# Performance work log

Measured on AMD Instinct MI355X. Metric: run time of the kernel, lower is better.

The kernel has to match this reference:

```python
import jax, jax.numpy as jnp
import numpy as np

B, H, W, CIN = 16, 64, 64, 64
KWH, COUT, NSAMPLE = 3, 128, 8


def setup_inputs() -> dict:
    key = jax.random.key(0)
    k1, k2, k3, k4 = jax.random.split(key, 4)
    x = jax.random.normal(k1, (B, H, W, CIN), dtype=jnp.float32)
    mu = jax.random.normal(k2, (KWH, KWH, CIN, COUT), dtype=jnp.float32)
    logstd = jax.random.normal(k3, (KWH, KWH, CIN, COUT), dtype=jnp.float32)
    noise = jax.random.normal(k4, (NSAMPLE, KWH, KWH, CIN, COUT), dtype=jnp.float32)
    return {"x": x, "mu": mu, "logstd": logstd, "noise": noise}


def reference(x, mu, logstd, noise):
    # Sampled kernels: [nsample, kh, kw, cin, cout]
    kernels = mu[None] + noise * jnp.exp(logstd)[None]

    def conv_one(k):
        y = jax.lax.conv_general_dilated(
            x, k, window_strides=(1, 1), padding='SAME',
            dimension_numbers=('NHWC', 'HWIO', 'NHWC'))
        return jax.nn.elu(y)

    # [nsample, B, H, W, cout] -> [B, H, W, nsample, cout]
    out = jax.vmap(conv_one)(kernels)
    return jnp.transpose(out, (1, 2, 3, 0, 4))
```

## Files before the change

### kernel.cpp

```cpp
#include <hip/hip_runtime.h>
#include <hip/hip_bf16.h>

typedef __attribute__((ext_vector_type(8))) short short8;
typedef __attribute__((ext_vector_type(8))) unsigned short ushort8;
typedef __attribute__((ext_vector_type(4))) float floatx4;

#define AS_STRIDE 72

#define KERF_BYTES (1024 * 576 * 2)

__global__ void prep_k(const float* __restrict__ x,
                       const float* __restrict__ mu,
                       const float* __restrict__ logstd,
                       const float* __restrict__ noise,
                       __hip_bfloat16* __restrict__ kerF,
                       __hip_bfloat16* __restrict__ xpad) {
  const int bx = blockIdx.x;
  const int tid = threadIdx.x;
  if (bx >= 72) {
    int i = (bx - 72) * 256 + tid;
    int row = i >> 3, seg = i & 7;
    int b = row / 4356;
    int rem = row - b * 4356;
    int hp = rem / 66, wp = rem - (rem / 66) * 66;
    int h = hp - 1, w = wp - 1;
    ushort8 val = {0, 0, 0, 0, 0, 0, 0, 0};
    if ((unsigned)h < 64u && (unsigned)w < 64u) {
      const float* src = x + ((((size_t)b * 64 + h) * 64 + w) << 6) + (seg << 3);
      float4 v0 = *(const float4*)src;
      float4 v1 = *(const float4*)(src + 4);
      val[0] = __bfloat16_as_ushort(__float2bfloat16(v0.x));
      val[1] = __bfloat16_as_ushort(__float2bfloat16(v0.y));
      val[2] = __bfloat16_as_ushort(__float2bfloat16(v0.z));
      val[3] = __bfloat16_as_ushort(__float2bfloat16(v0.w));
      val[4] = __bfloat16_as_ushort(__float2bfloat16(v1.x));
      val[5] = __bfloat16_as_ushort(__float2bfloat16(v1.y));
      val[6] = __bfloat16_as_ushort(__float2bfloat16(v1.z));
      val[7] = __bfloat16_as_ushort(__float2bfloat16(v1.w));
    }
    *(ushort8*)(xpad + ((size_t)row << 6) + (seg << 3)) = val;
  } else {
    const int s = bx / 9, tap = bx % 9;
    const float* mu_p = mu + tap * 8192;
    const float* ls_p = logstd + tap * 8192;
    const float* nz_p = noise + (s * 9 + tap) * 8192;
    for (int f = tid; f < 1024; f += 256) {
      int khalf = f >> 9;
      int nz = (f >> 6) & 7;
      int lane = f & 63;
      int co = ((nz >> 2) << 6) + (lane & 15) * 4 + (nz & 3);
      int ci0 = khalf * 32 + ((lane >> 4) & 3) * 8;
      short8 frag;
#pragma unroll
      for (int j = 0; j < 8; ++j) {
        int idx = (ci0 + j) * 128 + co;
        float v = mu_p[idx] + nz_p[idx] * expf(ls_p[idx]);
        frag[j] = (short)__bfloat16_as_ushort(__float2bfloat16(v));
      }
      *(short8*)(kerF + ((size_t)((s * 18 + tap * 2 + khalf) * 8 + nz) * 64 + lane) * 8) = frag;
    }
  }
}

__global__ __launch_bounds__(256, 3)
void conv_elu_k(const __hip_bfloat16* __restrict__ xpad,
                const __hip_bfloat16* __restrict__ kerF,
                float* __restrict__ out) {
  __shared__ __hip_bfloat16 As[4 * 66 * AS_STRIDE];

  const int tid = threadIdx.x;
  const int lane = tid & 63;
  const int lane15 = tid & 15;
  const int quad = (tid >> 4) & 3;
  const int wave = tid >> 6;
  const int n_tile = blockIdx.x & 7;
  const int mt_base = blockIdx.x >> 3;

  const int row_sel = wave >> 1;
  const int nz0sel = wave & 1;

  const __hip_bfloat16* bBase =
      kerF + (size_t)n_tile * 18 * 8 * 64 * 8 + (nz0sel << 2) * 512 + lane * 8;
  const __hip_bfloat16* aRowBase =
      As + (row_sel * 66 + lane15) * AS_STRIDE + quad * 8;

  short8 aE[4], aO[4], bE[4], bO[4];

  auto loadB = [&](short8* dst, const __hip_bfloat16* p) {
#pragma unroll
    for (int ni = 0; ni < 4; ++ni)
      dst[ni] = *(const short8*)(p + ni * 512);
  };
  auto loadA = [&](short8* dst, const __hip_bfloat16* row, int khalfOff) {
#pragma unroll
    for (int mi = 0; mi < 4; ++mi)
      dst[mi] = *(const short8*)(row + khalfOff + mi * 16 * AS_STRIDE);
  };

#pragma unroll 1
  for (int it = 0; it < 4; ++it) {
    const int mt = mt_base + (it << 7);
    const int b = mt >> 5;
    const int h0 = (mt & 31) << 1;

    const __hip_bfloat16* xbase = xpad + (((size_t)(b * 66 + h0) * 66) << 6);
    for (int c = tid; c < 2112; c += 256) {
      ushort8 v = *(const ushort8*)(xbase + ((size_t)c << 3));
      int r = c / 528;
      int cc = c - r * 528;
      int j = cc >> 3;
      int ci = (cc & 7) << 3;
      *(ushort8*)&As[(r * 66 + j) * AS_STRIDE + ci] = v;
    }

    floatx4 acc[4][4] = {};
    const __hip_bfloat16* bPtr = bBase;
    const __hip_bfloat16* aRow = aRowBase;

    __syncthreads();

    auto mfmaStep = [&](short8 (&a)[4], short8 (&bb)[4]) {
#pragma unroll
      for (int mi = 0; mi < 4; ++mi)
#pragma unroll
        for (int ni = 0; ni < 4; ++ni)
          acc[mi][ni] = __builtin_amdgcn_mfma_f32_16x16x32_bf16(
              a[mi], bb[ni], acc[mi][ni], 0, 0, 0);
    };

    loadB(bE, bPtr);
    loadA(aE, aRow, 0);
    int kw = 0;
#pragma unroll 1
    for (int tap = 0; tap < 8; ++tap) {
      loadB(bO, bPtr + 4096);
      loadA(aO, aRow, 32);
      mfmaStep(aE, bE);
      bPtr += 8192;
      aRow += AS_STRIDE;
      if (++kw == 3) { kw = 0; aRow += 63 * AS_STRIDE; }
      loadB(bE, bPtr);
      loadA(aE, aRow, 0);
      mfmaStep(aO, bO);
    }
    loadB(bO, bPtr + 4096);
    loadA(aO, aRow, 32);
    mfmaStep(aE, bE);
    mfmaStep(aO, bO);

    const int h = h0 + row_sel;
    float* outp = out + (size_t)((b * 64 + h) * 64) * 1024 +
                  (size_t)(n_tile * 128 + (nz0sel << 6) + (lane15 << 2));
#pragma unroll
    for (int mi = 0; mi < 4; ++mi) {
#pragma unroll
      for (int r = 0; r < 4; ++r) {
        int w = mi * 16 + quad * 4 + r;
        float4 v;
        float e0 = acc[mi][0][r];
        float e1 = acc[mi][1][r];
        float e2 = acc[mi][2][r];
        float e3 = acc[mi][3][r];
        v.x = e0 > 0.f ? e0 : __expf(e0) - 1.f;
        v.y = e1 > 0.f ? e1 : __expf(e1) - 1.f;
        v.z = e2 > 0.f ? e2 : __expf(e2) - 1.f;
        v.w = e3 > 0.f ? e3 : __expf(e3) - 1.f;
        *(float4*)(outp + (size_t)w * 1024) = v;
      }
    }

    if (it < 3) __syncthreads();
  }
}

extern "C" void kernel_launch(void* const* d_in, const int* in_sizes, int n_in,
                              void* d_out, int out_size, void* d_ws, size_t ws_size,
                              hipStream_t stream) {
  const float* x      = (const float*)d_in[0];
  const float* mu     = (const float*)d_in[1];
  const float* logstd = (const float*)d_in[2];
  const float* noise  = (const float*)d_in[3];
  float* out = (float*)d_out;
  __hip_bfloat16* kerF = (__hip_bfloat16*)d_ws;
  __hip_bfloat16* xpad = (__hip_bfloat16*)((char*)d_ws + KERF_BYTES);

  prep_k<<<2250, 256, 0, stream>>>(x, mu, logstd, noise, kerF, xpad);
  conv_elu_k<<<1024, 256, 0, stream>>>(xpad, kerF, out);
}
```

Baseline: 341.5 us.

## Stage padded input tiles via global_load_lds and prefetch next tile under epilogue

The padded input buffer now stores each pixel with a 72-element stride, so a tile can be copied straight into LDS with direct global-to-LDS 16-byte loads and no register round trip or index remapping. The next tile's load is issued before the ELU/store epilogue so it overlaps with output writes. The B-fragment loop is rewritten with triple-buffered registers to prefetch B one half-tap further ahead. In exchange the prep kernel writes about 12% more bytes, the tile load moves more data including padding, and register pressure rises.

```diff
diff --git a/kernel.cpp b/kernel.cpp
--- a/kernel.cpp
+++ b/kernel.cpp
@@ -8,6 +8,8 @@
 #define AS_STRIDE 72
 
 #define KERF_BYTES (1024 * 576 * 2)
+#define XPAD_PIX (16 * 66 * 66)
+#define XPAD_SEGS (XPAD_PIX * 9)
 
 __global__ void prep_k(const float* __restrict__ x,
                        const float* __restrict__ mu,
@@ -19,26 +21,28 @@
   const int tid = threadIdx.x;
   if (bx >= 72) {
     int i = (bx - 72) * 256 + tid;
-    int row = i >> 3, seg = i & 7;
-    int b = row / 4356;
-    int rem = row - b * 4356;
-    int hp = rem / 66, wp = rem - (rem / 66) * 66;
-    int h = hp - 1, w = wp - 1;
-    ushort8 val = {0, 0, 0, 0, 0, 0, 0, 0};
-    if ((unsigned)h < 64u && (unsigned)w < 64u) {
-      const float* src = x + ((((size_t)b * 64 + h) * 64 + w) << 6) + (seg << 3);
-      float4 v0 = *(const float4*)src;
-      float4 v1 = *(const float4*)(src + 4);
-      val[0] = __bfloat16_as_ushort(__float2bfloat16(v0.x));
-      val[1] = __bfloat16_as_ushort(__float2bfloat16(v0.y));
-      val[2] = __bfloat16_as_ushort(__float2bfloat16(v0.z));
-      val[3] = __bfloat16_as_ushort(__float2bfloat16(v0.w));
-      val[4] = __bfloat16_as_ushort(__float2bfloat16(v1.x));
-      val[5] = __bfloat16_as_ushort(__float2bfloat16(v1.y));
-      val[6] = __bfloat16_as_ushort(__float2bfloat16(v1.z));
-      val[7] = __bfloat16_as_ushort(__float2bfloat16(v1.w));
-    }
-    *(ushort8*)(xpad + ((size_t)row << 6) + (seg << 3)) = val;
+    if (i < XPAD_SEGS) {
+      int pixel = i / 9, seg = i - (i / 9) * 9;
+      int b = pixel / 4356;
+      int rem = pixel - b * 4356;
+      int hp = rem / 66, wp = rem - (rem / 66) * 66;
+      int h = hp - 1, w = wp - 1;
+      ushort8 val = {0, 0, 0, 0, 0, 0, 0, 0};
+      if (seg < 8 && (unsigned)h < 64u && (unsigned)w < 64u) {
+        const float* src = x + ((((size_t)b * 64 + h) * 64 + w) << 6) + (seg << 3);
+        float4 v0 = *(const float4*)src;
+        float4 v1 = *(const float4*)(src + 4);
+        val[0] = __bfloat16_as_ushort(__float2bfloat16(v0.x));
+        val[1] = __bfloat16_as_ushort(__float2bfloat16(v0.y));
+        val[2] = __bfloat16_as_ushort(__float2bfloat16(v0.z));
+        val[3] = __bfloat16_as_ushort(__float2bfloat16(v0.w));
+        val[4] = __bfloat16_as_ushort(__float2bfloat16(v1.x));
+        val[5] = __bfloat16_as_ushort(__float2bfloat16(v1.y));
+        val[6] = __bfloat16_as_ushort(__float2bfloat16(v1.z));
+        val[7] = __bfloat16_as_ushort(__float2bfloat16(v1.w));
+      }
+      *(ushort8*)(xpad + (size_t)i * 8) = val;
+    }
   } else {
     const int s = bx / 9, tap = bx % 9;
     const float* mu_p = mu + tap * 8192;
@@ -62,11 +66,17 @@
   }
 }
 
+__device__ inline void gll16(const void* g, void* l) {
+  __builtin_amdgcn_global_load_lds(
+      (const __attribute__((address_space(1))) unsigned int*)g,
+      (__attribute__((address_space(3))) unsigned int*)l, 16, 0, 0);
+}
+
 __global__ __launch_bounds__(256, 3)
 void conv_elu_k(const __hip_bfloat16* __restrict__ xpad,
                 const __hip_bfloat16* __restrict__ kerF,
                 float* __restrict__ out) {
-  __shared__ __hip_bfloat16 As[4 * 66 * AS_STRIDE];
+  __shared__ __hip_bfloat16 As[20480];
 
   const int tid = threadIdx.x;
   const int lane = tid & 63;
@@ -84,7 +94,7 @@
   const __hip_bfloat16* aRowBase =
       As + (row_sel * 66 + lane15) * AS_STRIDE + quad * 8;
 
-  short8 aE[4], aO[4], bE[4], bO[4];
+  short8 aE[4], aO[4], bA[4], bB[4], bC[4];
 
   auto loadB = [&](short8* dst, const __hip_bfloat16* p) {
 #pragma unroll
@@ -96,6 +106,20 @@
     for (int mi = 0; mi < 4; ++mi)
       dst[mi] = *(const short8*)(row + khalfOff + mi * 16 * AS_STRIDE);
   };
+
+  auto stage = [&](int it) {
+    const int mtN = mt_base + (it << 7);
+    const int bN = mtN >> 5;
+    const int h0N = (mtN & 31) << 1;
+    const __hip_bfloat16* g = xpad + (size_t)((bN * 66 + h0N) * 66) * AS_STRIDE;
+#pragma unroll
+    for (int c0 = 0; c0 < 2560; c0 += 256) {
+      int c = c0 + tid;
+      gll16(g + (size_t)c * 8, (void*)(As + (size_t)(c0 + (tid & 192)) * 8));
+    }
+  };
+
+  stage(0);
 
 #pragma unroll 1
   for (int it = 0; it < 4; ++it) {
@@ -103,21 +127,12 @@
     const int b = mt >> 5;
     const int h0 = (mt & 31) << 1;
 
-    const __hip_bfloat16* xbase = xpad + (((size_t)(b * 66 + h0) * 66) << 6);
-    for (int c = tid; c < 2112; c += 256) {
-      ushort8 v = *(const ushort8*)(xbase + ((size_t)c << 3));
-      int r = c / 528;
-      int cc = c - r * 528;
-      int j = cc >> 3;
-      int ci = (cc & 7) << 3;
-      *(ushort8*)&As[(r * 66 + j) * AS_STRIDE + ci] = v;
-    }
+    __syncthreads();
 
     floatx4 acc[4][4] = {};
     const __hip_bfloat16* bPtr = bBase;
     const __hip_bfloat16* aRow = aRowBase;
-
-    __syncthreads();
+    int kw = 0;
 
     auto mfmaStep = [&](short8 (&a)[4], short8 (&bb)[4]) {
 #pragma unroll
@@ -128,25 +143,34 @@
               a[mi], bb[ni], acc[mi][ni], 0, 0, 0);
     };
 
-    loadB(bE, bPtr);
-    loadA(aE, aRow, 0);
-    int kw = 0;
-#pragma unroll 1
-    for (int tap = 0; tap < 8; ++tap) {
-      loadB(bO, bPtr + 4096);
+    auto TAP = [&](short8 (&bEv)[4], short8 (&bOd)[4], short8 (&bNx)[4],
+                   bool last) {
+      if (!last) loadB(bNx, bPtr + 8192);
       loadA(aO, aRow, 32);
-      mfmaStep(aE, bE);
+      mfmaStep(aE, bEv);
       bPtr += 8192;
       aRow += AS_STRIDE;
       if (++kw == 3) { kw = 0; aRow += 63 * AS_STRIDE; }
-      loadB(bE, bPtr);
-      loadA(aE, aRow, 0);
-      mfmaStep(aO, bO);
-    }
-    loadB(bO, bPtr + 4096);
-    loadA(aO, aRow, 32);
-    mfmaStep(aE, bE);
-    mfmaStep(aO, bO);
+      if (!last) {
+        loadB(bEv, bPtr + 4096);
+        loadA(aE, aRow, 0);
+      }
+      mfmaStep(aO, bOd);
+    };
+
+    loadB(bA, bPtr);
+    loadB(bB, bPtr + 4096);
+    loadA(aE, aRow, 0);
+#pragma unroll 1
+    for (int t3 = 0; t3 < 3; ++t3) {
+      TAP(bA, bB, bC, false);
+      TAP(bC, bA, bB, false);
+      TAP(bB, bC, bA, t3 == 2);
+    }
+
+    __syncthreads();
+
+    if (it < 3) stage(it + 1);
 
     const int h = h0 + row_sel;
     float* outp = out + (size_t)((b * 64 + h) * 64) * 1024 +
@@ -168,8 +192,6 @@
         *(float4*)(outp + (size_t)w * 1024) = v;
       }
     }
-
-    if (it < 3) __syncthreads();
   }
 }
 
@@ -184,6 +206,6 @@
   __hip_bfloat16* kerF = (__hip_bfloat16*)d_ws;
   __hip_bfloat16* xpad = (__hip_bfloat16*)((char*)d_ws + KERF_BYTES);
 
-  prep_k<<<2250, 256, 0, stream>>>(x, mu, logstd, noise, kerF, xpad);
+  prep_k<<<72 + 2451, 256, 0, stream>>>(x, mu, logstd, noise, kerF, xpad);
   conv_elu_k<<<1024, 256, 0, stream>>>(xpad, kerF, out);
 }
```

Measured after the change: 383.3 us. +12.2%, slower.
